# Optimization experiments

Hardware: AMD Instinct MI355X
Metric: run time of the kernel (lower is better)

## Reference

```python
import jax, jax.numpy as jnp
import numpy as np

MEDNUM = 50000
FEATDIM = 128
NNZ = 3200000
N = 2 * MEDNUM  # adjacency is over cat([mEmbed, mEmbed])


def setup_inputs() -> dict:
    key = jax.random.key(0)
    k1, k2, k3, k4, k5 = jax.random.split(key, 5)
    vals = jax.random.uniform(k1, (NNZ,), dtype=jnp.float32)
    mEmbed = jax.random.normal(k2, (MEDNUM, FEATDIM), dtype=jnp.float32)
    inter = jax.random.normal(k3, (1,), dtype=jnp.float32)
    row_idx = jax.random.randint(k4, (NNZ,), 0, N, dtype=jnp.int32)
    col_idx = jax.random.randint(k5, (NNZ,), 0, N, dtype=jnp.int32)
    return {"vals": vals, "mEmbed": mEmbed, "inter": inter,
            "row_idx": row_idx, "col_idx": col_idx}


def _gcn_layer(vals, row_idx, col_idx, embeds):
    # spmm(adj, embeds) via gather + weighted segment-sum, then LeakyReLU(0.5)
    gathered = embeds[col_idx] * vals[:, None]          # [E, F]
    agg = jax.ops.segment_sum(gathered, row_idx, num_segments=N)  # [N, F]
    return jnp.where(agg >= 0, agg, 0.5 * agg)          # LeakyReLU(negative_slope=0.5)


def reference(vals, mEmbed, inter, row_idx, col_idx):
    embeds1 = jnp.concatenate([mEmbed, mEmbed], axis=0)  # [2*mednum, F]
    # Source quirk: lats1 is never extended, so both iterations use embeds1.
    tem1 = jax.nn.relu(_gcn_layer(vals, row_idx, col_idx, embeds1))
    gnnEmbeds1 = tem1 + tem1                              # sum of two identical layers
    m1 = gnnEmbeds1[:MEDNUM]
    m2 = gnnEmbeds1[MEDNUM:]
    return inter * m1 + (1.0 - inter) * m2
```

## Files before the change

kernel.cpp:

```cpp
#include <hip/hip_runtime.h>

#define MEDNUM 50000
#define FEATDIM 128
#define NNZ 3200000
#define NBUCK 1563
#define SLAB 2304
#define PART_BLOCKS 250
#define PART_E 12800
#define PART_K 25
#define CAP SLAB

#define OFF_CUR    0
#define OFF_SCALE  1600
#define OFF_QT     51600
#define OFF_RECS   3251600

__global__ __launch_bounds__(256) void toint8_kernel(const float* __restrict__ mEmbed,
                                                     unsigned short* __restrict__ qt,
                                                     float* __restrict__ scales,
                                                     int* __restrict__ gcur) {
    int g = blockIdx.x * 256 + threadIdx.x;
    if (g < NBUCK) gcur[g] = g * SLAB;

    int row = blockIdx.x * 4 + (threadIdx.x >> 6);
    int lane = threadIdx.x & 63;
    if (row >= MEDNUM) return;
    float2 f = ((const float2*)(mEmbed + (long long)row * FEATDIM))[lane];
    float m = fmaxf(fabsf(f.x), fabsf(f.y));
    for (int o = 32; o > 0; o >>= 1) m = fmaxf(m, __shfl_xor(m, o, 64));
    float inv = (m > 0.f) ? 127.f / m : 0.f;
    float s   = (m > 0.f) ? m / 127.f : 0.f;
    int q0 = __float2int_rn(f.x * inv) + 128;
    int q1 = __float2int_rn(f.y * inv) + 128;
    qt[(long long)row * 64 + lane] =
        (unsigned short)((q0 & 0xff) | ((q1 & 0xff) << 8));
    if (lane == 0) scales[row] = s;
}

__global__ __launch_bounds__(512, 2) void part_kernel(const float* __restrict__ vals,
                                                      const int* __restrict__ row_idx,
                                                      const int* __restrict__ col_idx,
                                                      const float* __restrict__ scales,
                                                      int* __restrict__ gcur,
                                                      unsigned long long* __restrict__ recs) {
    __shared__ unsigned long long lrec[PART_E];
    __shared__ int lcnt[NBUCK];
    __shared__ int gstart[NBUCK];
    __shared__ int wsum[8];

    int tid = threadIdx.x;
    int base = blockIdx.x * PART_E;

    for (int i = tid; i < NBUCK; i += 512) lcnt[i] = 0;
    __syncthreads();

    unsigned long long rec[PART_K];
    {
        int rr[PART_K], cc[PART_K];
        float vv[PART_K];
#pragma unroll
        for (int k = 0; k < PART_K; k++) {
            int e = base + k * 512 + tid;
            rr[k] = __builtin_nontemporal_load(row_idx + e);
            cc[k] = __builtin_nontemporal_load(col_idx + e);
            vv[k] = __builtin_nontemporal_load(vals + e);
        }
        float ss[PART_K];
#pragma unroll
        for (int k = 0; k < PART_K; k++) {
            cc[k] = (cc[k] >= MEDNUM) ? cc[k] - MEDNUM : cc[k];
            ss[k] = scales[cc[k]];
        }
#pragma unroll
        for (int k = 0; k < PART_K; k++) {
            int r = rr[k], half = 0;
            if (r >= MEDNUM) { r -= MEDNUM; half = 1; }
            float vp = vv[k] * ss[k];
            int b = r >> 5;
            int rib = (r & 31) | (half << 5);
            rec[k] = ((unsigned long long)__float_as_uint(vp) << 32)
                   | ((unsigned long long)(b >> 10) << 63)
                   | ((unsigned int)(b & 0x3FF) << 22)
                   | ((unsigned int)rib << 16)
                   | (unsigned int)cc[k];
            atomicAdd(&lcnt[b], 1);
        }
    }
    __syncthreads();

    int i0 = tid * 4;
    int c0 = 0, c1 = 0, c2 = 0, c3 = 0;
    if (i0 < NBUCK)     c0 = lcnt[i0];
    if (i0 + 1 < NBUCK) c1 = lcnt[i0 + 1];
    if (i0 + 2 < NBUCK) c2 = lcnt[i0 + 2];
    if (i0 + 3 < NBUCK) c3 = lcnt[i0 + 3];
    int s = c0 + c1 + c2 + c3;
    int x = s;
#pragma unroll
    for (int d = 1; d < 64; d <<= 1) {
        int t = __shfl_up(x, d, 64);
        if ((tid & 63) >= d) x += t;
    }
    int wave = tid >> 6, lane = tid & 63;
    if (lane == 63) wsum[wave] = x;
    __syncthreads();
    if (tid == 0) {
        int acc = 0;
#pragma unroll
        for (int w = 0; w < 8; w++) { int t = wsum[w]; wsum[w] = acc; acc += t; }
    }
    __syncthreads();
    int excl = wsum[wave] + x - s;

    {
        int e = excl;
        int cs[4] = {c0, c1, c2, c3};
#pragma unroll
        for (int q = 0; q < 4; q++) {
            int i = i0 + q;
            if (i < NBUCK) {
                int c = cs[q];
                if (c > 0) {
                    int gb = atomicAdd(&gcur[i], c);
                    gstart[i] = gb - e;
                }
                lcnt[i] = e;
                e += c;
            }
        }
    }
    __syncthreads();

#pragma unroll
    for (int k = 0; k < PART_K; k++) {
        unsigned long long r = rec[k];
        int b = (int)(((r >> 53) & 0x400u) | ((r >> 22) & 0x3FFu));
        int pos = atomicAdd(&lcnt[b], 1);
        lrec[pos] = r;
    }
    __syncthreads();

#pragma unroll
    for (int k = 0; k < PART_K; k++) {
        int j = k * 512 + tid;
        unsigned long long r = lrec[j];
        int b = (int)(((r >> 53) & 0x400u) | ((r >> 22) & 0x3FFu));
        int addr = gstart[b] + j;
        recs[addr] = r & 0x7FFFFFFFFFFFFFFFULL;
    }
}

__device__ __forceinline__ void accum4_body(const unsigned int p[4],
                                            const unsigned short* __restrict__ qt,
                                            unsigned int flo,
                                            float acc[8], float& sv) {
#pragma unroll
    for (int q = 0; q < 4; q++) {
        unsigned int off = ((p[q] & 0xffffu) << 7) | flo;
        unsigned long long w = *(const unsigned long long*)((const char*)qt + off);
        float v = __uint_as_float(p[q] & 0xffff0000u);
        sv += v;
        unsigned int wlo = (unsigned int)w, whi = (unsigned int)(w >> 32);
        acc[0] = fmaf(v, (float)(wlo & 0xffu),         acc[0]);
        acc[1] = fmaf(v, (float)((wlo >> 8) & 0xffu),  acc[1]);
        acc[2] = fmaf(v, (float)((wlo >> 16) & 0xffu), acc[2]);
        acc[3] = fmaf(v, (float)(wlo >> 24),           acc[3]);
        acc[4] = fmaf(v, (float)(whi & 0xffu),         acc[4]);
        acc[5] = fmaf(v, (float)((whi >> 8) & 0xffu),  acc[5]);
        acc[6] = fmaf(v, (float)((whi >> 16) & 0xffu), acc[6]);
        acc[7] = fmaf(v, (float)(whi >> 24),           acc[7]);
    }
}

__device__ __forceinline__ void accum_seg4(int s, int e,
                                           const unsigned int* __restrict__ st4,
                                           const unsigned short* __restrict__ qt,
                                           int qw, unsigned int flo,
                                           float acc[8], float& sv) {
#pragma unroll
    for (int x = 0; x < 8; x++) acc[x] = 0.f;
    sv = 0.f;
    int i = s;
    for (; i + 16 <= e; i += 16) {
        unsigned int p[4];
#pragma unroll
        for (int q = 0; q < 4; q++) p[q] = st4[i + q * 4 + qw];
        accum4_body(p, qt, flo, acc, sv);
    }
    if (i < e) {
        unsigned int p[4];
#pragma unroll
        for (int q = 0; q < 4; q++) {
            int j = i + q * 4 + qw;
            p[q] = (j < e) ? st4[j] : 0u;
        }
        accum4_body(p, qt, flo, acc, sv);
    }
}

__global__ __launch_bounds__(512, 8) void agg_kernel(const int* __restrict__ gcur,
                                                     const unsigned long long* __restrict__ recs,
                                                     const unsigned short* __restrict__ qt,
                                                     const float* __restrict__ inter,
                                                     float* __restrict__ out) {
    __shared__ unsigned int st4[CAP];
    __shared__ int cnt[64];
    __shared__ int bas[65];
    int b = blockIdx.x, tid = threadIdx.x;
    long long gs = (long long)b * SLAB;
    int n = gcur[b] - b * SLAB;
    if (n > CAP) n = CAP;

    if (tid < 64) cnt[tid] = 0;
    __syncthreads();
    unsigned long long rl[5];
#pragma unroll
    for (int k = 0; k < 5; k++) {
        int j = k * 512 + tid;
        if (j < n) rl[k] = recs[gs + j];
    }
#pragma unroll
    for (int k = 0; k < 5; k++) {
        int j = k * 512 + tid;
        if (j < n) atomicAdd(&cnt[(int)((rl[k] >> 16) & 63)], 1);
    }
    __syncthreads();
    if (tid < 64) {
        int v = cnt[tid];
        int x = v;
#pragma unroll
        for (int d = 1; d < 64; d <<= 1) {
            int tmp = __shfl_up(x, d, 64);
            if (tid >= d) x += tmp;
        }
        bas[tid] = x - v;
        if (tid == 63) bas[64] = x;
        cnt[tid] = x - v;
    }
    __syncthreads();
#pragma unroll
    for (int k = 0; k < 5; k++) {
        int j = k * 512 + tid;
        if (j < n) {
            unsigned long long r = rl[k];
            int rib = (int)((r >> 16) & 63);
            int p = atomicAdd(&cnt[rib], 1);
            unsigned int vb = (unsigned int)(r >> 32);
            vb = (vb + 0x7fffu + ((vb >> 16) & 1u)) & 0xffff0000u;
            st4[p] = ((unsigned int)(r & 0xffff)) | vb;
        }
    }
    __syncthreads();
    float t = inter[0];
    float s1 = 2.f * t, s2 = 2.f * (1.f - t);
    int wave = tid >> 6, lane = tid & 63;
    int qw = lane >> 4;
    unsigned int flo = (unsigned int)((lane & 15) << 3);
#pragma unroll 1
    for (int i2 = 0; i2 < 4; i2++) {
        int rib0 = wave * 4 + i2;
        int frow = b * 32 + rib0;
        if (frow >= MEDNUM) break;
        float a[8], c[8], sva, svc;
        accum_seg4(bas[rib0],      bas[rib0 + 1],  st4, qt, qw, flo, a, sva);
        accum_seg4(bas[rib0 + 32], bas[rib0 + 33], st4, qt, qw, flo, c, svc);
#pragma unroll
        for (int x2 = 0; x2 < 8; x2++) {
            a[x2] += __shfl_xor(a[x2], 16, 64);
            a[x2] += __shfl_xor(a[x2], 32, 64);
            c[x2] += __shfl_xor(c[x2], 16, 64);
            c[x2] += __shfl_xor(c[x2], 32, 64);
        }
        sva += __shfl_xor(sva, 16, 64); sva += __shfl_xor(sva, 32, 64);
        svc += __shfl_xor(svc, 16, 64); svc += __shfl_xor(svc, 32, 64);
        if (qw == 0) {
            float r[8];
#pragma unroll
            for (int x2 = 0; x2 < 8; x2++) {
                float av = fmaf(-128.f, sva, a[x2]);
                float cv = fmaf(-128.f, svc, c[x2]);
                r[x2] = s1 * fmaxf(av, 0.f) + s2 * fmaxf(cv, 0.f);
            }
            float* op = out + (long long)frow * FEATDIM + ((lane & 15) << 3);
            *(float4*)op       = make_float4(r[0], r[1], r[2], r[3]);
            *(float4*)(op + 4) = make_float4(r[4], r[5], r[6], r[7]);
        }
    }
}

extern "C" void kernel_launch(void* const* d_in, const int* in_sizes, int n_in,
                              void* d_out, int out_size, void* d_ws, size_t ws_size,
                              hipStream_t stream) {
    const float* vals    = (const float*)d_in[0];
    const float* mEmbed  = (const float*)d_in[1];
    const float* inter   = (const float*)d_in[2];
    const int*   row_idx = (const int*)d_in[3];
    const int*   col_idx = (const int*)d_in[4];
    float* out = (float*)d_out;

    int* ws = (int*)d_ws;
    int* gcur = ws + OFF_CUR;
    float* scales = (float*)(ws + OFF_SCALE);
    unsigned short* qt = (unsigned short*)(ws + OFF_QT);
    unsigned long long* recs = (unsigned long long*)(ws + OFF_RECS);

    toint8_kernel<<<(MEDNUM + 3) / 4, 256, 0, stream>>>(mEmbed, qt, scales, gcur);
    part_kernel<<<PART_BLOCKS, 512, 0, stream>>>(vals, row_idx, col_idx, scales, gcur, recs);
    agg_kernel<<<NBUCK, 512, 0, stream>>>(gcur, recs, qt, inter, out);
}
```

Before: 228.8 us.

## Interleave paired segment loops, permute int8 table, store output with all lanes

The two per-row segment accumulations (both halves of the concatenated graph) now run in one interleaved loop. Eight independent gathers are issued before any decoding, which raises memory-level parallelism. The quantized table is stored in a permuted column order so that after the cross-lane reduction every lane holds two consecutive output features. This replaces the qw==0-only float4 stores with coalesced float2 stores from all 64 lanes. The shorter segment now does predicated dummy iterations until the longer one finishes, and register pressure rises.

```diff
diff --git a/kernel.cpp b/kernel.cpp
--- a/kernel.cpp
+++ b/kernel.cpp
@@ -14,6 +14,7 @@
 #define OFF_SCALE  1600
 #define OFF_QT     51600
 #define OFF_RECS   3251600
+
 
 __global__ __launch_bounds__(256) void toint8_kernel(const float* __restrict__ mEmbed,
                                                      unsigned short* __restrict__ qt,
@@ -32,7 +33,7 @@
     float s   = (m > 0.f) ? m / 127.f : 0.f;
     int q0 = __float2int_rn(f.x * inv) + 128;
     int q1 = __float2int_rn(f.y * inv) + 128;
-    qt[(long long)row * 64 + lane] =
+    qt[(long long)row * 64 + ((lane & 15) * 4 + (lane >> 4))] =
         (unsigned short)((q0 & 0xff) | ((q1 & 0xff) << 8));
     if (lane == 0) scales[row] = s;
 }
@@ -150,51 +151,57 @@
     }
 }
 
-__device__ __forceinline__ void accum4_body(const unsigned int p[4],
-                                            const unsigned short* __restrict__ qt,
-                                            unsigned int flo,
-                                            float acc[8], float& sv) {
-#pragma unroll
-    for (int q = 0; q < 4; q++) {
-        unsigned int off = ((p[q] & 0xffffu) << 7) | flo;
-        unsigned long long w = *(const unsigned long long*)((const char*)qt + off);
-        float v = __uint_as_float(p[q] & 0xffff0000u);
-        sv += v;
-        unsigned int wlo = (unsigned int)w, whi = (unsigned int)(w >> 32);
-        acc[0] = fmaf(v, (float)(wlo & 0xffu),         acc[0]);
-        acc[1] = fmaf(v, (float)((wlo >> 8) & 0xffu),  acc[1]);
-        acc[2] = fmaf(v, (float)((wlo >> 16) & 0xffu), acc[2]);
-        acc[3] = fmaf(v, (float)(wlo >> 24),           acc[3]);
-        acc[4] = fmaf(v, (float)(whi & 0xffu),         acc[4]);
-        acc[5] = fmaf(v, (float)((whi >> 8) & 0xffu),  acc[5]);
-        acc[6] = fmaf(v, (float)((whi >> 16) & 0xffu), acc[6]);
-        acc[7] = fmaf(v, (float)(whi >> 24),           acc[7]);
-    }
-}
-
-__device__ __forceinline__ void accum_seg4(int s, int e,
+__device__ __forceinline__ void decode8(unsigned long long w, unsigned int p,
+                                        float acc[8], float& sv) {
+    float v = __uint_as_float(p & 0xffff0000u);
+    sv += v;
+    unsigned int wlo = (unsigned int)w, whi = (unsigned int)(w >> 32);
+    acc[0] = fmaf(v, (float)(wlo & 0xffu),         acc[0]);
+    acc[1] = fmaf(v, (float)((wlo >> 8) & 0xffu),  acc[1]);
+    acc[2] = fmaf(v, (float)((wlo >> 16) & 0xffu), acc[2]);
+    acc[3] = fmaf(v, (float)(wlo >> 24),           acc[3]);
+    acc[4] = fmaf(v, (float)(whi & 0xffu),         acc[4]);
+    acc[5] = fmaf(v, (float)((whi >> 8) & 0xffu),  acc[5]);
+    acc[6] = fmaf(v, (float)((whi >> 16) & 0xffu), acc[6]);
+    acc[7] = fmaf(v, (float)(whi >> 24),           acc[7]);
+}
+
+__device__ __forceinline__ void accum_pair(int a0, int a1, int b0, int b1,
                                            const unsigned int* __restrict__ st4,
                                            const unsigned short* __restrict__ qt,
                                            int qw, unsigned int flo,
-                                           float acc[8], float& sv) {
-#pragma unroll
-    for (int x = 0; x < 8; x++) acc[x] = 0.f;
-    sv = 0.f;
-    int i = s;
-    for (; i + 16 <= e; i += 16) {
-        unsigned int p[4];
-#pragma unroll
-        for (int q = 0; q < 4; q++) p[q] = st4[i + q * 4 + qw];
-        accum4_body(p, qt, flo, acc, sv);
-    }
-    if (i < e) {
-        unsigned int p[4];
+                                           float a[8], float c[8],
+                                           float& sva, float& svc) {
+#pragma unroll
+    for (int x = 0; x < 8; x++) { a[x] = 0.f; c[x] = 0.f; }
+    sva = 0.f; svc = 0.f;
+    int ia = a0, ib = b0;
+    while (ia < a1 || ib < b1) {
+        unsigned int pa[4], pb[4];
 #pragma unroll
         for (int q = 0; q < 4; q++) {
-            int j = i + q * 4 + qw;
-            p[q] = (j < e) ? st4[j] : 0u;
-        }
-        accum4_body(p, qt, flo, acc, sv);
+            int j = ia + q * 4 + qw;
+            pa[q] = (j < a1) ? st4[j] : 0u;
+        }
+#pragma unroll
+        for (int q = 0; q < 4; q++) {
+            int j = ib + q * 4 + qw;
+            pb[q] = (j < b1) ? st4[j] : 0u;
+        }
+        unsigned long long wa[4], wb[4];
+#pragma unroll
+        for (int q = 0; q < 4; q++)
+            wa[q] = *(const unsigned long long*)((const char*)qt
+                        + (((pa[q] & 0xffffu) << 7) | flo));
+#pragma unroll
+        for (int q = 0; q < 4; q++)
+            wb[q] = *(const unsigned long long*)((const char*)qt
+                        + (((pb[q] & 0xffffu) << 7) | flo));
+#pragma unroll
+        for (int q = 0; q < 4; q++) decode8(wa[q], pa[q], a, sva);
+#pragma unroll
+        for (int q = 0; q < 4; q++) decode8(wb[q], pb[q], c, svc);
+        ia += 16; ib += 16;
     }
 }
 
@@ -262,8 +269,8 @@
         int frow = b * 32 + rib0;
         if (frow >= MEDNUM) break;
         float a[8], c[8], sva, svc;
-        accum_seg4(bas[rib0],      bas[rib0 + 1],  st4, qt, qw, flo, a, sva);
-        accum_seg4(bas[rib0 + 32], bas[rib0 + 33], st4, qt, qw, flo, c, svc);
+        accum_pair(bas[rib0], bas[rib0 + 1], bas[rib0 + 32], bas[rib0 + 33],
+                   st4, qt, qw, flo, a, c, sva, svc);
 #pragma unroll
         for (int x2 = 0; x2 < 8; x2++) {
             a[x2] += __shfl_xor(a[x2], 16, 64);
@@ -273,18 +280,18 @@
         }
         sva += __shfl_xor(sva, 16, 64); sva += __shfl_xor(sva, 32, 64);
         svc += __shfl_xor(svc, 16, 64); svc += __shfl_xor(svc, 32, 64);
-        if (qw == 0) {
-            float r[8];
-#pragma unroll
-            for (int x2 = 0; x2 < 8; x2++) {
-                float av = fmaf(-128.f, sva, a[x2]);
-                float cv = fmaf(-128.f, svc, c[x2]);
-                r[x2] = s1 * fmaxf(av, 0.f) + s2 * fmaxf(cv, 0.f);
-            }
-            float* op = out + (long long)frow * FEATDIM + ((lane & 15) << 3);
-            *(float4*)op       = make_float4(r[0], r[1], r[2], r[3]);
-            *(float4*)(op + 4) = make_float4(r[4], r[5], r[6], r[7]);
-        }
+        float ax = (qw & 2) ? ((qw & 1) ? a[6] : a[4]) : ((qw & 1) ? a[2] : a[0]);
+        float ay = (qw & 2) ? ((qw & 1) ? a[7] : a[5]) : ((qw & 1) ? a[3] : a[1]);
+        float cx = (qw & 2) ? ((qw & 1) ? c[6] : c[4]) : ((qw & 1) ? c[2] : c[0]);
+        float cy = (qw & 2) ? ((qw & 1) ? c[7] : c[5]) : ((qw & 1) ? c[3] : c[1]);
+        float axc = fmaf(-128.f, sva, ax);
+        float ayc = fmaf(-128.f, sva, ay);
+        float cxc = fmaf(-128.f, svc, cx);
+        float cyc = fmaf(-128.f, svc, cy);
+        float2 o;
+        o.x = s1 * fmaxf(axc, 0.f) + s2 * fmaxf(cxc, 0.f);
+        o.y = s1 * fmaxf(ayc, 0.f) + s2 * fmaxf(cyc, 0.f);
+        *(float2*)(out + (long long)frow * FEATDIM + lane * 2) = o;
     }
 }
 
```

Measured after the change: 377.5 us. +65.0%, slower.
